# Performance work log

Measured on AMD Instinct MI355X. Metric: run time of the kernel, lower is better.

The kernel has to match this reference:

```python
import jax, jax.numpy as jnp
import numpy as np

B, S, DIM, H = 2, 2048, 1024, 16
DH = DIM // H            # 64
G = DH // 4              # 16 quaternion groups per head
IQ = DIM // 4            # 256
ROPE_BASE = 10000.0
SCALE = DH ** -0.5


def qlinear(x, wr, wi, wj, wk, b):
    # x: [B,S,4*IQ]; strided quaternion components, exact combo from QuaternionLinear.forward
    xr, xi, xj, xk = x[..., 0::4], x[..., 1::4], x[..., 2::4], x[..., 3::4]
    o_r = xr @ wr.T - xi @ wi.T - xj @ wj.T - xk @ wk.T
    o_i = xi @ wr.T + xr @ wi.T + xk @ wk.T - xj @ wj.T
    o_j = xj @ wr.T - xk @ wk.T + xr @ wj.T + xi @ wi.T
    o_k = xk @ wr.T + xj @ wj.T - xi @ wi.T + xr @ wk.T
    out = jnp.stack([o_r, o_i, o_j, o_k], axis=-1).reshape(x.shape[:-1] + (-1,))
    return out + b


def qrope(x):
    # x: [B,H,S,DH]; left quaternion multiply u(theta) \otimes q, axis_mode='cycle'
    b, h, s, dh = x.shape
    g = dh // 4
    xq = x.reshape(b, h, s, g, 4)
    t = jnp.arange(s, dtype=x.dtype)
    inv = 1.0 / (ROPE_BASE ** (jnp.arange(g, dtype=x.dtype) / g))
    ang = t[:, None] * inv[None, :]            # [S,G]
    cos, sin = jnp.cos(ang), jnp.sin(ang)
    gi = jnp.arange(g)
    ax_i = (gi % 3 == 0).astype(x.dtype)
    ax_j = (gi % 3 == 1).astype(x.dtype)
    ax_k = (gi % 3 == 2).astype(x.dtype)
    ur, ui, uj, uk = cos, sin * ax_i, sin * ax_j, sin * ax_k   # [S,G] broadcast over [B,H,S,G]
    xr, xi, xj, xk = xq[..., 0], xq[..., 1], xq[..., 2], xq[..., 3]
    pr = ur * xr - ui * xi - uj * xj - uk * xk
    pi = ur * xi + ui * xr + uj * xk - uk * xj
    pj = ur * xj - ui * xk + uj * xr + uk * xi
    pk = ur * xk + ui * xj - uj * xi + uk * xr
    return jnp.stack([pr, pi, pj, pk], axis=-1).reshape(b, h, s, dh)


def setup_inputs() -> dict:
    key = jax.random.key(0)
    ks = jax.random.split(key, 24)
    x = jax.random.normal(ks[0], (B, S, DIM), dtype=jnp.float32)
    # causal mask: True = masked
    mask = jnp.broadcast_to(jnp.triu(jnp.ones((S, S), dtype=bool), k=1), (B, S, S))
    inp = {"x": x, "mask": mask}
    i = 1
    for proj in ("q", "k", "v", "o"):
        for comp in ("wr", "wi", "wj", "wk"):
            inp[f"{proj}_{comp}"] = jax.random.normal(ks[i], (IQ, IQ), dtype=jnp.float32) * 0.02
            i += 1
        inp[f"{proj}_b"] = jnp.zeros((DIM,), dtype=jnp.float32)
    return inp


def reference(x, mask,
              q_wr, q_wi, q_wj, q_wk, q_b,
              k_wr, k_wi, k_wj, k_wk, k_b,
              v_wr, v_wi, v_wj, v_wk, v_b,
              o_wr, o_wi, o_wj, o_wk, o_b):
    b, s, dm = x.shape
    q = qlinear(x, q_wr, q_wi, q_wj, q_wk, q_b).reshape(b, s, H, DH).transpose(0, 2, 1, 3)
    k = qlinear(x, k_wr, k_wi, k_wj, k_wk, k_b).reshape(b, s, H, DH).transpose(0, 2, 1, 3)
    v = qlinear(x, v_wr, v_wi, v_wj, v_wk, v_b).reshape(b, s, H, DH).transpose(0, 2, 1, 3)
    q, k = qrope(q), qrope(k)
    scores = jnp.einsum('bhsd,bhtd->bhst', q, k) * SCALE
    scores = jnp.where(mask[:, None, :, :], -jnp.inf, scores)
    a = jax.nn.softmax(scores, axis=-1)
    out = jnp.einsum('bhst,bhtd->bhsd', a, v).transpose(0, 2, 1, 3).reshape(b, s, dm)
    return qlinear(out, o_wr, o_wi, o_wj, o_wk, o_b)
```

## Files before the change

kernel.cpp:

```cpp
#include <hip/hip_runtime.h>
#include <stdint.h>

typedef unsigned short u16;
typedef unsigned int   u32;

#define NB   2
#define NS   2048
#define NDIM 1024
#define NH   16
#define NDH  64
#define QSCALE 0.18033688011112042f

typedef __bf16 bf16x8 __attribute__((ext_vector_type(8)));
typedef float  f32x4  __attribute__((ext_vector_type(4)));

#define MFMA_BF16(a,b,c) __builtin_amdgcn_mfma_f32_16x16x32_bf16((a),(b),(c),0,0,0)

#define XBF_OFF   (256)
#define WD_OFF    (XBF_OFF  + 8*1024*1024)
#define BIAS_OFF  (WD_OFF   + 8*1024*1024)
#define QB_OFF    (BIAS_OFF + 16384)
#define KB_OFF    (QB_OFF   + 8*1024*1024)
#define VT_OFF    (KB_OFF   + 8*1024*1024)
#define OP_OFF    (VT_OFF   + 8*1024*1024)
#define LP_OFF    (OP_OFF   + 16*1024*1024)

__device__ __forceinline__ float bf2f(u16 h){
  union { u32 u; float f; } v; v.u = ((u32)h) << 16; return v.f;
}
__device__ __forceinline__ u16 f2bf(float f){
  union { float f; u32 u; } v; v.f = f;
  u32 r = (v.u >> 16) & 1u;
  return (u16)((v.u + 0x7fffu + r) >> 16);
}
__device__ __forceinline__ float load_val(const void* p, int i, int isbf){
  return isbf ? bf2f(((const u16*)p)[i]) : ((const float*)p)[i];
}
__device__ __forceinline__ void gl_lds16(const u16* g, u16* l){
  __builtin_amdgcn_global_load_lds(
      (__attribute__((address_space(1))) void*)(uintptr_t)g,
      (__attribute__((address_space(3))) void*)(uintptr_t)l,
      16, 0, 0);
}

__global__ void detect_kernel(const u16* __restrict__ x, int* __restrict__ flag){
  __shared__ int cnt;
  if (threadIdx.x == 0) cnt = 0;
  __syncthreads();
  int ok = 0;
  int base = threadIdx.x * 16;
  for (int i = base; i < base + 16; ++i){
    u16 h = x[i];
    int e = (h >> 7) & 0xFF;
    if ((e > 96 && e < 158) || ((h & 0x7FFF) == 0)) ok++;
  }
  atomicAdd(&cnt, ok);
  __syncthreads();
  if (threadIdx.x == 0) *flag = (cnt > 3600) ? 1 : 0;
}

__global__ void conv_x_kernel(const void* __restrict__ xin, u16* __restrict__ xbf,
                              const int* __restrict__ flag){
  int isbf = *flag;
  int t = blockIdx.x * 256 + threadIdx.x;
  if (isbf){
    ((uint4*)xbf)[t] = ((const uint4*)xin)[t];
  } else {
    const float4* f4 = (const float4*)xin;
    float4 a = f4[2*t], b = f4[2*t+1];
    ushort4 lo = { f2bf(a.x), f2bf(a.y), f2bf(a.z), f2bf(a.w) };
    ushort4 hi = { f2bf(b.x), f2bf(b.y), f2bf(b.z), f2bf(b.w) };
    ((ushort4*)xbf)[2*t]   = lo;
    ((ushort4*)xbf)[2*t+1] = hi;
  }
}

struct QPtrs { const void* w[16]; const void* b[4]; };

__global__ void build_w_kernel(QPtrs ptrs, u16* __restrict__ wd,
                               float* __restrict__ biasf, const int* __restrict__ flag){
  int isbf = *flag;
  int idx = blockIdx.x * 256 + threadIdx.x;
  int n = idx & 255, m = (idx >> 8) & 255, c = (idx >> 16) & 3, p = idx >> 18;
  int src = m * 256 + n;
  float vr = load_val(ptrs.w[p*4+0], src, isbf);
  float vi = load_val(ptrs.w[p*4+1], src, isbf);
  float vj = load_val(ptrs.w[p*4+2], src, isbf);
  float vk = load_val(ptrs.w[p*4+3], src, isbf);
  float o0, o1, o2, o3;
  switch (c){
    case 0:  o0 = vr; o1 = -vi; o2 = -vj; o3 = -vk; break;
    case 1:  o0 = vi; o1 =  vr; o2 = -vj; o3 =  vk; break;
    case 2:  o0 = vj; o1 =  vi; o2 =  vr; o3 = -vk; break;
    default: o0 = vk; o1 = -vi; o2 =  vj; o3 =  vr; break;
  }
  ushort4 sv = { f2bf(o0), f2bf(o1), f2bf(o2), f2bf(o3) };
  *(ushort4*)&wd[(size_t)p * 1048576 + (size_t)(4*m + c) * 1024 + 4*n] = sv;
  if (idx < 4096){
    int pp = idx >> 10, oo = idx & 1023;
    biasf[idx] = load_val(ptrs.b[pp], oo, isbf);
  }
}

__global__ __launch_bounds__(256)
void gemm_qkv_kernel(const u16* __restrict__ A, const u16* __restrict__ Bw,
                     const float* __restrict__ bias,
                     u16* __restrict__ qb, u16* __restrict__ kb, u16* __restrict__ vt){
  __shared__ u16 sA[2][128 * 32];
  __shared__ u16 sB[2][128 * 32];
  int tid = threadIdx.x, w = tid >> 6, lane = tid & 63, quad = lane >> 4, l16 = lane & 15;
  int n0 = blockIdx.x * 128, m0 = blockIdx.y * 128;

  f32x4 acc[4][4];
#pragma unroll
  for (int i = 0; i < 4; ++i)
#pragma unroll
    for (int j = 0; j < 4; ++j) acc[i][j] = (f32x4){0.f, 0.f, 0.f, 0.f};

  int cp = lane & 3, rl = lane >> 2;
  int gc = (cp ^ ((rl >> 1) & 3)) * 8;
  const u16* ga = A  + (size_t)(m0 + w*16 + rl) * 1024 + gc;
  const u16* gb = Bw + (size_t)(n0 + w*16 + rl) * 1024 + gc;
  int ldo = w * 512 + lane * 8;
  int xorv = ((l16 >> 1) & 3) * 8;
  int mw = (w & 1) * 64, nw = (w >> 1) * 64;

  auto stage = [&](int k0, int b){
#pragma unroll
    for (int i = 0; i < 2; ++i){
      gl_lds16(ga + (size_t)i * 65536 + k0, &sA[b][ldo + i * 2048]);
      gl_lds16(gb + (size_t)i * 65536 + k0, &sB[b][ldo + i * 2048]);
    }
  };

  stage(0, 0);
  for (int it = 0; it < 32; ++it){
    __syncthreads();
    if (it < 31) stage((it + 1) * 32, (it + 1) & 1);
    const u16* cA = sA[it & 1];
    const u16* cB = sB[it & 1];
    bf16x8 af[4], bfr[4];
#pragma unroll
    for (int mt = 0; mt < 4; ++mt)
      af[mt] = *(const bf16x8*)&cA[(mw + mt*16 + l16) * 32 + (quad*8 ^ xorv)];
#pragma unroll
    for (int nt = 0; nt < 4; ++nt)
      bfr[nt] = *(const bf16x8*)&cB[(nw + nt*16 + l16) * 32 + (quad*8 ^ xorv)];
#pragma unroll
    for (int mt = 0; mt < 4; ++mt)
#pragma unroll
      for (int nt = 0; nt < 4; ++nt)
        acc[mt][nt] = MFMA_BF16(af[mt], bfr[nt], acc[mt][nt]);
  }

  int proj = n0 >> 10;
  if (proj == 2){
#pragma unroll
    for (int mt = 0; mt < 4; ++mt){
      int row = m0 + mw + mt*16 + quad*4;
      int b = row >> 11, seq0 = row & 2047;
#pragma unroll
      for (int nt = 0; nt < 4; ++nt){
        int col = n0 + nw + nt*16 + l16;
        int o = col & 1023, h = o >> 6, d = o & 63;
        float bv = bias[col];
        ushort4 pv = { f2bf(acc[mt][nt][0] + bv), f2bf(acc[mt][nt][1] + bv),
                       f2bf(acc[mt][nt][2] + bv), f2bf(acc[mt][nt][3] + bv) };
        *(ushort4*)&vt[((size_t)((b*16 + h) * 64 + d)) * 2048 + seq0] = pv;
      }
    }
  } else {
    float sc = (proj == 0) ? QSCALE : 1.0f;
    u16* dst = proj ? kb : qb;
    int c = l16 & 3;
#pragma unroll
    for (int nt = 0; nt < 4; ++nt){
      int col = n0 + nw + nt*16 + l16;
      int o = col & 1023, h = o >> 6, d = o & 63;
      int g = d >> 2;
      int ax = g % 3;
      int mask = ax + 1;
      int tbl = (ax == 0) ? 0xA : (ax == 1 ? 0x6 : 0xC);
      float sgn = ((tbl >> c) & 1) ? 1.f : -1.f;
      float inv = __builtin_amdgcn_exp2f(-(float)g * 0.8304820237218405f);
      float bv = bias[col];
#pragma unroll
      for (int mt = 0; mt < 4; ++mt){
        int row0 = m0 + mw + mt*16 + quad*4;
        int b = row0 >> 11, s0 = row0 & 2047;
        size_t obase = ((size_t)((b*16 + h) * 2048 + s0)) * 64 + d;
#pragma unroll
        for (int r = 0; r < 4; ++r){
          float v = acc[mt][nt][r] + bv;
          float vp = __shfl_xor(v, mask);
          float ang = (float)(s0 + r) * inv;
          float co = __cosf(ang) * sc;
          float si = __sinf(ang) * sc * sgn;
          dst[obase + (size_t)r * 64] = f2bf(co * v + si * vp);
        }
      }
    }
  }
}

__global__ __launch_bounds__(256)
void gemm_o_kernel(const u16* __restrict__ A, const u16* __restrict__ Bw,
                   const float* __restrict__ bias, void* __restrict__ dout,
                   const int* __restrict__ flag){
  __shared__ u16 sA[2][64 * 32];
  __shared__ u16 sB[2][128 * 32];
  int tid = threadIdx.x, w = tid >> 6, lane = tid & 63, quad = lane >> 4, l16 = lane & 15;
  int n0 = blockIdx.x * 128, m0 = blockIdx.y * 64;

  f32x4 acc[2][4];
#pragma unroll
  for (int i = 0; i < 2; ++i)
#pragma unroll
    for (int j = 0; j < 4; ++j) acc[i][j] = (f32x4){0.f, 0.f, 0.f, 0.f};

  int cp = lane & 3, rl = lane >> 2;
  int gc = (cp ^ ((rl >> 1) & 3)) * 8;
  int xorv = ((l16 >> 1) & 3) * 8;
  int mw = (w & 1) * 32, nw = (w >> 1) * 64;

  auto stage = [&](int k0, int b){
#pragma unroll
    for (int i = 0; i < 3; ++i){
      int ch = w * 3 + i;
      int lr = (ch < 4 ? ch : ch - 4) * 16 + rl;
      int eo = (ch < 4 ? ch : ch - 4) * 512 + lane * 8;
      if (ch < 4) gl_lds16(A  + (size_t)(m0 + lr) * 1024 + k0 + gc, &sA[b][eo]);
      else        gl_lds16(Bw + (size_t)(n0 + lr) * 1024 + k0 + gc, &sB[b][eo]);
    }
  };

  stage(0, 0);
  for (int it = 0; it < 32; ++it){
    __syncthreads();
    if (it < 31) stage((it + 1) * 32, (it + 1) & 1);
    const u16* cA = sA[it & 1];
    const u16* cB = sB[it & 1];
    bf16x8 af[2], bfr[4];
#pragma unroll
    for (int mt = 0; mt < 2; ++mt)
      af[mt] = *(const bf16x8*)&cA[(mw + mt*16 + l16) * 32 + (quad*8 ^ xorv)];
#pragma unroll
    for (int nt = 0; nt < 4; ++nt)
      bfr[nt] = *(const bf16x8*)&cB[(nw + nt*16 + l16) * 32 + (quad*8 ^ xorv)];
#pragma unroll
    for (int mt = 0; mt < 2; ++mt)
#pragma unroll
      for (int nt = 0; nt < 4; ++nt)
        acc[mt][nt] = MFMA_BF16(af[mt], bfr[nt], acc[mt][nt]);
  }

  int isbf = *flag;
#pragma unroll
  for (int mt = 0; mt < 2; ++mt){
    int row = m0 + mw + mt*16 + quad*4;
#pragma unroll
    for (int nt = 0; nt < 4; ++nt){
      int col = n0 + nw + nt*16 + l16;
      float bv = bias[col];
#pragma unroll
      for (int r = 0; r < 4; ++r){
        float val = acc[mt][nt][r] + bv;
        size_t addr = (size_t)(row + r) * 1024 + col;
        if (isbf) ((u16*)dout)[addr] = f2bf(val);
        else      ((float*)dout)[addr] = val;
      }
    }
  }
}

#define SPT 20

__global__ __launch_bounds__(256, 3)
void attn_kernel(const u16* __restrict__ Q, const u16* __restrict__ K,
                 const u16* __restrict__ Vt, u16* __restrict__ OP,
                 float* __restrict__ LP){
  __shared__ u16 sK[2][4096];
  __shared__ u16 sPT[4][64 * SPT];
  int bh  = blockIdx.x;
  int spl = blockIdx.y;
  int qt  = 15 - (int)blockIdx.z;
  int tid = threadIdx.x, w = tid >> 6, lane = tid & 63, quad = lane >> 4, l16 = lane & 15;
  size_t kbase = (size_t)bh * 2048 * 64;
  size_t vbase = (size_t)bh * 64 * 2048;
  int rowbase = qt * 128 + w * 32;
  u16* spw = &sPT[w][0];

  bf16x8 qf[2][2];
#pragma unroll
  for (int g = 0; g < 2; ++g)
#pragma unroll
    for (int kc = 0; kc < 2; ++kc)
      qf[g][kc] = *(const bf16x8*)(Q + kbase + (size_t)(rowbase + g*16 + l16) * 64 + kc*32 + quad*8);

  f32x4 oaccT[2][4];
  float lsum[2][4];
#pragma unroll
  for (int g = 0; g < 2; ++g)
#pragma unroll
    for (int i = 0; i < 4; ++i){ oaccT[g][i] = (f32x4){0.f,0.f,0.f,0.f}; lsum[g][i] = 0.f; }

  int kt0 = spl ? (qt + 1) : 0;
  int ntiles = qt + 1;

  auto stage = [&](int kt, int b){
    int kcol = kt * 64;
#pragma unroll
    for (int p = 0; p < 2; ++p){
      int slot = w*128 + p*64 + lane;
      int row = slot >> 3, dc = (slot & 7) ^ (row & 7);
      gl_lds16(K + kbase + (size_t)(kcol + row) * 64 + dc*8, &sK[b][(w*128 + p*64) * 8]);
    }
  };

  stage(kt0, 0);
  for (int i = 0; i < ntiles; ++i){
    int kcol = (kt0 + i) * 64;
    __syncthreads();
    if (i + 1 < ntiles) stage(kt0 + i + 1, (i + 1) & 1);
    const u16* bK = sK[i & 1];

    if (kcol <= rowbase + 31){
      bf16x8 vf[4][2];
#pragma unroll
      for (int dn = 0; dn < 4; ++dn)
#pragma unroll
        for (int kc = 0; kc < 2; ++kc)
          vf[dn][kc] = *(const bf16x8*)(Vt + vbase + (size_t)(dn*16 + l16) * 2048
                                        + kcol + kc*32 + quad*8);
      bf16x8 bk[2][4];
#pragma unroll
      for (int kc = 0; kc < 2; ++kc)
#pragma unroll
        for (int nt = 0; nt < 4; ++nt){
          int rw = nt*16 + l16;
          int ch = ((kc*4 + quad) ^ (rw & 7)) * 8;
          bk[kc][nt] = *(const bf16x8*)&bK[rw*64 + ch];
        }
#pragma unroll
      for (int g = 0; g < 2; ++g){
        int G0 = rowbase + g*16;
        if (kcol <= G0 + 15){
          f32x4 sacc[4];
#pragma unroll
          for (int nt = 0; nt < 4; ++nt) sacc[nt] = (f32x4){0.f,0.f,0.f,0.f};
#pragma unroll
          for (int kc = 0; kc < 2; ++kc)
#pragma unroll
            for (int nt = 0; nt < 4; ++nt)
              sacc[nt] = MFMA_BF16(qf[g][kc], bk[kc][nt], sacc[nt]);

          if (kcol + 63 > G0){
#pragma unroll
            for (int nt = 0; nt < 4; ++nt){
              int col = kcol + nt*16 + l16;
              ushort4 pv;
#pragma unroll
              for (int r = 0; r < 4; ++r){
                int row = G0 + quad*4 + r;
                float pp = (col <= row) ? __builtin_amdgcn_exp2f(sacc[nt][r]) : 0.f;
                lsum[g][r] += pp;
                ((u16*)&pv)[r] = f2bf(pp);
              }
              *(ushort4*)&spw[(nt*16 + l16) * SPT + quad*4] = pv;
            }
          } else {
#pragma unroll
            for (int nt = 0; nt < 4; ++nt){
              ushort4 pv;
#pragma unroll
              for (int r = 0; r < 4; ++r){
                float pp = __builtin_amdgcn_exp2f(sacc[nt][r]);
                lsum[g][r] += pp;
                ((u16*)&pv)[r] = f2bf(pp);
              }
              *(ushort4*)&spw[(nt*16 + l16) * SPT + quad*4] = pv;
            }
          }
#pragma unroll
          for (int kc = 0; kc < 2; ++kc){
            bf16x8 pf;
#pragma unroll
            for (int j = 0; j < 8; ++j)
              pf[j] = ((const __bf16*)spw)[(kc*32 + quad*8 + j) * SPT + l16];
#pragma unroll
            for (int dn = 0; dn < 4; ++dn)
              oaccT[g][dn] = MFMA_BF16(vf[dn][kc], pf, oaccT[g][dn]);
          }
        }
      }
    }
  }

  float* scr = (float*)spw;
#pragma unroll
  for (int g = 0; g < 2; ++g)
#pragma unroll
    for (int r = 0; r < 4; ++r){
      float l = lsum[g][r];
      l += __shfl_xor(l, 1); l += __shfl_xor(l, 2);
      l += __shfl_xor(l, 4); l += __shfl_xor(l, 8);
      if (l16 == 0) scr[g*16 + quad*4 + r] = l;
    }
  float lrow[2];
#pragma unroll
  for (int g = 0; g < 2; ++g) lrow[g] = scr[g*16 + l16];

  size_t obase = ((size_t)(spl*32 + bh)) * 2048;
#pragma unroll
  for (int g = 0; g < 2; ++g){
    int row = rowbase + g*16 + l16;
    if (quad == 0) LP[obase + row] = lrow[g];
#pragma unroll
    for (int dn = 0; dn < 4; ++dn){
      ushort4 ov = { f2bf(oaccT[g][dn][0]), f2bf(oaccT[g][dn][1]),
                     f2bf(oaccT[g][dn][2]), f2bf(oaccT[g][dn][3]) };
      *(ushort4*)&OP[(obase + row) * 64 + dn*16 + quad*4] = ov;
    }
  }
}

__global__ void combine_kernel(const u16* __restrict__ OP, const float* __restrict__ LP,
                               u16* __restrict__ Ab){
  int idx = blockIdx.x * 256 + threadIdx.x;
  int dc = idx & 7, s = (idx >> 3) & 2047, bh = idx >> 14;
  size_t r0 = (size_t)bh * 2048 + s, r1 = (size_t)(32 + bh) * 2048 + s;
  float invl = 1.f / (LP[r0] + LP[r1]);
  union { uint4 v; u16 h[8]; } a0, a1; ushort4 o[2];
  a0.v = *(const uint4*)&OP[r0 * 64 + dc*8];
  a1.v = *(const uint4*)&OP[r1 * 64 + dc*8];
#pragma unroll
  for (int p = 0; p < 2; ++p)
#pragma unroll
    for (int j = 0; j < 4; ++j)
      ((u16*)&o[p])[j] = f2bf((bf2f(a0.h[p*4+j]) + bf2f(a1.h[p*4+j])) * invl);
  int b = bh >> 4, h = bh & 15;
  u16* dst = &Ab[((size_t)(b*2048 + s)) * 1024 + h*64 + dc*8];
  *(ushort4*)dst = o[0];
  *(ushort4*)(dst + 4) = o[1];
}

extern "C" void kernel_launch(void* const* d_in, const int* in_sizes, int n_in,
                              void* d_out, int out_size, void* d_ws, size_t ws_size,
                              hipStream_t stream){
  (void)in_sizes; (void)n_in; (void)out_size; (void)ws_size;
  char* ws = (char*)d_ws;
  int*   flag  = (int*)ws;
  u16*   Xbf   = (u16*)(ws + XBF_OFF);
  u16*   Wd    = (u16*)(ws + WD_OFF);
  float* biasf = (float*)(ws + BIAS_OFF);
  u16*   Qb    = (u16*)(ws + QB_OFF);
  u16*   Kb    = (u16*)(ws + KB_OFF);
  u16*   Vt    = (u16*)(ws + VT_OFF);
  u16*   OP    = (u16*)(ws + OP_OFF);
  float* LP    = (float*)(ws + LP_OFF);
  u16*   Ab    = Xbf;

  detect_kernel<<<1, 256, 0, stream>>>((const u16*)d_in[0], flag);
  conv_x_kernel<<<2048, 256, 0, stream>>>(d_in[0], Xbf, flag);

  QPtrs ptrs;
  for (int p = 0; p < 4; ++p){
    for (int wi = 0; wi < 4; ++wi) ptrs.w[p*4 + wi] = d_in[2 + p*5 + wi];
    ptrs.b[p] = d_in[2 + p*5 + 4];
  }
  build_w_kernel<<<4096, 256, 0, stream>>>(ptrs, Wd, biasf, flag);

  gemm_qkv_kernel<<<dim3(24, 32), 256, 0, stream>>>(Xbf, Wd, biasf, Qb, Kb, Vt);
  attn_kernel<<<dim3(32, 2, 16), 256, 0, stream>>>(Qb, Kb, Vt, OP, LP);
  combine_kernel<<<2048, 256, 0, stream>>>(OP, LP, Ab);
  gemm_o_kernel<<<dim3(8, 64), 256, 0, stream>>>(Ab, Wd + 3*1048576, biasf + 3072,
                                                 d_out, flag);
}
```

Measured before the change: 251.1 us.

## Triple-buffer LDS staging in QKV and output GEMMs with explicit vmcnt waits

```diff
diff --git a/kernel.cpp b/kernel.cpp
--- a/kernel.cpp
+++ b/kernel.cpp
@@ -106,8 +106,8 @@
 void gemm_qkv_kernel(const u16* __restrict__ A, const u16* __restrict__ Bw,
                      const float* __restrict__ bias,
                      u16* __restrict__ qb, u16* __restrict__ kb, u16* __restrict__ vt){
-  __shared__ u16 sA[2][128 * 32];
-  __shared__ u16 sB[2][128 * 32];
+  __shared__ u16 sA[3][128 * 32];
+  __shared__ u16 sB[3][128 * 32];
   int tid = threadIdx.x, w = tid >> 6, lane = tid & 63, quad = lane >> 4, l16 = lane & 15;
   int n0 = blockIdx.x * 128, m0 = blockIdx.y * 128;
 
@@ -134,11 +134,15 @@
   };
 
   stage(0, 0);
+  stage(32, 1);
+  asm volatile("s_waitcnt vmcnt(4)" ::: "memory");
+  __builtin_amdgcn_s_barrier();
+
+  int bcur = 0, bnxt = 2;
   for (int it = 0; it < 32; ++it){
-    __syncthreads();
-    if (it < 31) stage((it + 1) * 32, (it + 1) & 1);
-    const u16* cA = sA[it & 1];
-    const u16* cB = sB[it & 1];
+    if (it < 30) stage((it + 2) * 32, bnxt);
+    const u16* cA = sA[bcur];
+    const u16* cB = sB[bcur];
     bf16x8 af[4], bfr[4];
 #pragma unroll
     for (int mt = 0; mt < 4; ++mt)
@@ -151,6 +155,12 @@
 #pragma unroll
       for (int nt = 0; nt < 4; ++nt)
         acc[mt][nt] = MFMA_BF16(af[mt], bfr[nt], acc[mt][nt]);
+
+    if (it < 30) asm volatile("s_waitcnt vmcnt(4)" ::: "memory");
+    else         asm volatile("s_waitcnt vmcnt(0)" ::: "memory");
+    __builtin_amdgcn_s_barrier();
+    bcur = (bcur == 2) ? 0 : bcur + 1;
+    bnxt = (bnxt == 2) ? 0 : bnxt + 1;
   }
 
   int proj = n0 >> 10;
@@ -207,8 +217,8 @@
 void gemm_o_kernel(const u16* __restrict__ A, const u16* __restrict__ Bw,
                    const float* __restrict__ bias, void* __restrict__ dout,
                    const int* __restrict__ flag){
-  __shared__ u16 sA[2][64 * 32];
-  __shared__ u16 sB[2][128 * 32];
+  __shared__ u16 sA[3][64 * 32];
+  __shared__ u16 sB[3][128 * 32];
   int tid = threadIdx.x, w = tid >> 6, lane = tid & 63, quad = lane >> 4, l16 = lane & 15;
   int n0 = blockIdx.x * 128, m0 = blockIdx.y * 64;
 
@@ -235,11 +245,15 @@
   };
 
   stage(0, 0);
+  stage(32, 1);
+  asm volatile("s_waitcnt vmcnt(3)" ::: "memory");
+  __builtin_amdgcn_s_barrier();
+
+  int bcur = 0, bnxt = 2;
   for (int it = 0; it < 32; ++it){
-    __syncthreads();
-    if (it < 31) stage((it + 1) * 32, (it + 1) & 1);
-    const u16* cA = sA[it & 1];
-    const u16* cB = sB[it & 1];
+    if (it < 30) stage((it + 2) * 32, bnxt);
+    const u16* cA = sA[bcur];
+    const u16* cB = sB[bcur];
     bf16x8 af[2], bfr[4];
 #pragma unroll
     for (int mt = 0; mt < 2; ++mt)
@@ -252,6 +266,12 @@
 #pragma unroll
       for (int nt = 0; nt < 4; ++nt)
         acc[mt][nt] = MFMA_BF16(af[mt], bfr[nt], acc[mt][nt]);
+
+    if (it < 30) asm volatile("s_waitcnt vmcnt(3)" ::: "memory");
+    else         asm volatile("s_waitcnt vmcnt(0)" ::: "memory");
+    __builtin_amdgcn_s_barrier();
+    bcur = (bcur == 2) ? 0 : bcur + 1;
+    bnxt = (bnxt == 2) ? 0 : bnxt + 1;
   }
 
   int isbf = *flag;
```

New measurement: 244.1 us. -2.8%, faster.
